# Kernel optimization log

Measured on AMD Instinct MI355X. Metric: run time of the kernel, lower is better.

Reference implementation:

```python
import jax, jax.numpy as jnp
import numpy as np


def setup_inputs() -> dict:
    key = jax.random.key(0)
    k = jax.random.split(key, 6)
    B, S, L, V = 512, 256, 128, 32000
    words = jax.random.randint(k[0], (B, S), 0, V)
    encoder_emits = jax.random.normal(k[1], (B, S, L), dtype=jnp.float32)
    mask = jnp.ones((B, S), dtype=bool)  # token 0 always valid; all-valid lengths here
    feature_table = jax.random.normal(k[2], (V, L), dtype=jnp.float32)
    start = jax.random.normal(k[3], (L,), dtype=jnp.float32)
    transitions = jax.random.normal(k[4], (L, L), dtype=jnp.float32)
    end = jax.random.normal(k[5], (L,), dtype=jnp.float32)
    return {"words": words, "encoder_emits": encoder_emits, "mask": mask,
            "feature_table": feature_table, "start": start,
            "transitions": transitions, "end": end}


def reference(words, encoder_emits, mask, feature_table, start, transitions, end):
    # decoder emits: feature_scorer(words) modeled as per-word label-score lookup
    dec = feature_table[words]                       # [B, S, L]
    # init at t = 0
    log_alpha = start[None, :] + encoder_emits[:, 0]  # [B, L]
    log_beta = log_alpha + dec[:, 0]                  # [B, L]

    def step(carry, xs):
        la, lb = carry
        e_i, d_i, m_i = xs                            # [B,L], [B,L], [B]
        crf = e_i[:, None, :] + transitions[None]     # [B, L, L] (prev, cur)
        a_new = jax.nn.logsumexp(la[:, :, None] + crf, axis=1)
        b_new = jax.nn.logsumexp(lb[:, :, None] + crf + d_i[:, None, :], axis=1)
        m = m_i[:, None]
        return (jnp.where(m, a_new, la), jnp.where(m, b_new, lb)), None

    xs = (jnp.swapaxes(encoder_emits[:, 1:], 0, 1),   # [S-1, B, L]
          jnp.swapaxes(dec[:, 1:], 0, 1),
          mask[:, 1:].T)                              # [S-1, B]
    (log_alpha, log_beta), _ = jax.lax.scan(step, (log_alpha, log_beta), xs)

    la = jax.nn.logsumexp(log_alpha + end[None, :], axis=-1)  # [B]
    lb = jax.nn.logsumexp(log_beta + end[None, :], axis=-1)   # [B]
    return (la - lb).sum()
```

## Files before the change

### kernel.cpp

```cpp
#include <hip/hip_runtime.h>


constexpr int SS  = 256;
constexpr int LL  = 128;
constexpr int BST = 136;

typedef _Float16 half2_t __attribute__((ext_vector_type(2)));
typedef _Float16 half4_t __attribute__((ext_vector_type(4)));
typedef _Float16 half8_t __attribute__((ext_vector_type(8)));
typedef float    f32x4   __attribute__((ext_vector_type(4)));
typedef unsigned uint2_t __attribute__((ext_vector_type(2)));

#define MFMA16(a, b, c) __builtin_amdgcn_mfma_f32_16x16x32_f16((a), (b), (c), 0, 0, 0)
#define PKRTZ(a, b) __builtin_bit_cast(half2_t, __builtin_amdgcn_cvt_pkrtz((a), (b)))

#define BAR() do {                                                \
    asm volatile("s_waitcnt lgkmcnt(0)" ::: "memory");            \
    __builtin_amdgcn_s_barrier();                                 \
    asm volatile("" ::: "memory");                                \
} while (0)

__device__ __forceinline__ float quad_allmax(float x) {
#if __has_builtin(__builtin_amdgcn_permlane16_swap) && __has_builtin(__builtin_amdgcn_permlane32_swap)
    unsigned u = __builtin_bit_cast(unsigned, x);
    uint2_t a = __builtin_amdgcn_permlane16_swap(u, u, false, false);
    float m = fmaxf(__builtin_bit_cast(float, a.x), __builtin_bit_cast(float, a.y));
    unsigned v = __builtin_bit_cast(unsigned, m);
    uint2_t b = __builtin_amdgcn_permlane32_swap(v, v, false, false);
    return fmaxf(__builtin_bit_cast(float, b.x), __builtin_bit_cast(float, b.y));
#else
    x = fmaxf(x, __shfl_xor(x, 16, 64));
    return fmaxf(x, __shfl_xor(x, 32, 64));
#endif
}

__global__ __launch_bounds__(256) void prepass(
    const int* __restrict__ words, const float* __restrict__ emits,
    const float* __restrict__ ftab,
    half4_t* __restrict__ xe, half4_t* __restrict__ xb,
    float* __restrict__ out)
{
    if (blockIdx.x == 0 && threadIdx.x == 0) *out = 0.f;
    const int t = threadIdx.x;
    const int R = blockIdx.x * 8 + (t >> 5);
    const int c = t & 31;
    const int w = words[R];
    const f32x4 e = *(const f32x4*)&emits[(size_t)R * LL + 4 * c];
    const f32x4 d = *(const f32x4*)&ftab[(size_t)w * LL + 4 * c];
    half4_t a, bb;
    #pragma unroll
    for (int r = 0; r < 4; ++r) {
        a[r]  = (_Float16)__expf(e[r]);
        bb[r] = (_Float16)__expf(e[r] + d[r]);
    }
    xe[(size_t)R * 32 + c] = a;
    xb[(size_t)R * 32 + c] = bb;
}

#define STEP(i, XS) do {                                                      \
    const int rp_ = ((i) + 1) & 1, wp_ = (i) & 1;                             \
    O2 -= __log2f(invp);             \
    half8_t bf_[4];                                                           \
    _Pragma("unroll")                                                         \
    for (int c = 0; c < 4; ++c)                                               \
        bf_[c] = *(const half8_t*)&P[rp_][m15 * BST + c * 32 + quad * 8];     \
    f32x4 a0_ = MFMA16(areg[0][0], bf_[0], zero4);                            \
    f32x4 b0_ = MFMA16(areg[0][2], bf_[2], zero4);                            \
    f32x4 a1_ = MFMA16(areg[1][0], bf_[0], zero4);                            \
    f32x4 b1_ = MFMA16(areg[1][2], bf_[2], zero4);                            \
    a0_ = MFMA16(areg[0][1], bf_[1], a0_);                                    \
    b0_ = MFMA16(areg[0][3], bf_[3], b0_);                                    \
    a1_ = MFMA16(areg[1][1], bf_[1], a1_);                                    \
    b1_ = MFMA16(areg[1][3], bf_[3], b1_);                                    \
    const f32x4 y0_ = a0_ + b0_;                                              \
    const f32x4 y1_ = a1_ + b1_;                                              \
    const float p0_ = y0_[0] * (float)XS[0][0] * invp;                        \
    const float p1_ = y0_[1] * (float)XS[0][1] * invp;                        \
    const float p2_ = y0_[2] * (float)XS[0][2] * invp;                        \
    const float p3_ = y0_[3] * (float)XS[0][3] * invp;                        \
    const float q0_ = y1_[0] * (float)XS[1][0] * invp;                        \
    const float q1_ = y1_[1] * (float)XS[1][1] * invp;                        \
    const float q2_ = y1_[2] * (float)XS[1][2] * invp;                        \
    const float q3_ = y1_[3] * (float)XS[1][3] * invp;                        \
    {                                                                         \
        half2_t h0_ = PKRTZ(p0_, p1_), h1_ = PKRTZ(p2_, p3_);                 \
        half4_t pa_; pa_[0]=h0_[0]; pa_[1]=h0_[1]; pa_[2]=h1_[0]; pa_[3]=h1_[1];\
        *(half4_t*)&P[wp_][m15 * BST + t0 * 16 + col0] = pa_;                 \
        half2_t g0_ = PKRTZ(q0_, q1_), g1_ = PKRTZ(q2_, q3_);                 \
        half4_t pb_; pb_[0]=g0_[0]; pb_[1]=g0_[1]; pb_[2]=g1_[0]; pb_[3]=g1_[1];\
        *(half4_t*)&P[wp_][m15 * BST + (t0 + 1) * 16 + col0] = pb_;           \
    }                                                                         \
    const int ipf_ = ((i) + 3 < SS) ? (i) + 3 : SS - 1;                       \
    XS[0] = *(const half4_t*)&X[xrow + (size_t)ipf_ * LL + t0 * 16 + col0];   \
    XS[1] = *(const half4_t*)&X[xrow + (size_t)ipf_ * LL + (t0+1) * 16 + col0];\
    float mm_ = fmaxf(fmaxf(fmaxf(p0_, p1_), fmaxf(p2_, p3_)),               \
                      fmaxf(fmaxf(q0_, q1_), fmaxf(q2_, q3_)));               \
    mm_ = quad_allmax(mm_);                                                   \
    if (quad == 0) PM[wp_][m15][wave] = mm_;                                  \
    BAR();                                                                    \
    const f32x4 pm_ = *(const f32x4*)&PM[wp_][m15][0];                        \
    invp = __builtin_amdgcn_rcpf(fmaxf(fmaxf(pm_[0], pm_[1]),                 \
                                       fmaxf(pm_[2], pm_[3])));               \
} while (0)

__global__ __launch_bounds__(256, 1) void crf_scan(
    const float* __restrict__ start,
    const float* __restrict__ trans,
    const float* __restrict__ endv,
    const _Float16* __restrict__ xe,
    const _Float16* __restrict__ xb,
    float* __restrict__ out)
{
    const int blk   = blockIdx.x;
    const int chain = blk & 1;
    const int grp   = blk >> 1;
    const int tid   = threadIdx.x;
    const int wave  = tid >> 6;
    const int lane  = tid & 63;
    const int m15   = lane & 15;
    const int quad  = lane >> 4;
    const int col0  = quad * 4;
    const int batch = grp * 16 + m15;
    const int t0    = wave * 2;
    const _Float16* __restrict__ X = chain ? xb : xe;

    __shared__ __align__(16) _Float16 P[2][16 * BST];
    __shared__ __align__(16) float    PM[2][16][4];

    half8_t areg[2][4];
    #pragma unroll
    for (int u = 0; u < 2; ++u)
        #pragma unroll
        for (int c = 0; c < 4; ++c)
            #pragma unroll
            for (int jj = 0; jj < 8; ++jj)
                areg[u][c][jj] = (_Float16)__expf(
                    trans[(c * 32 + quad * 8 + jj) * LL + (t0 + u) * 16 + m15]);

    const size_t xrow = (size_t)batch * SS * LL;
    const f32x4 zero4 = (f32x4){0.f, 0.f, 0.f, 0.f};

    float invp, O2 = 0.f;

    {
        float mm = -3.0e38f;
        #pragma unroll
        for (int u = 0; u < 2; ++u) {
            const int s0 = (t0 + u) * 16 + col0;
            const f32x4  sv = *(const f32x4*)&start[s0];
            const half4_t x0 = *(const half4_t*)&X[xrow + s0];
            float y0 = __expf(sv[0]) * (float)x0[0];
            float y1 = __expf(sv[1]) * (float)x0[1];
            float y2 = __expf(sv[2]) * (float)x0[2];
            float y3 = __expf(sv[3]) * (float)x0[3];
            half2_t h0 = PKRTZ(y0, y1), h1 = PKRTZ(y2, y3);
            half4_t pa; pa[0]=h0[0]; pa[1]=h0[1]; pa[2]=h1[0]; pa[3]=h1[1];
            *(half4_t*)&P[0][m15 * BST + s0] = pa;
            mm = fmaxf(mm, fmaxf(fmaxf(y0, y1), fmaxf(y2, y3)));
        }
        mm = quad_allmax(mm);
        if (quad == 0) PM[0][m15][wave] = mm;
    }
    BAR();
    {
        const f32x4 pm = *(const f32x4*)&PM[0][m15][0];
        invp = __builtin_amdgcn_rcpf(fmaxf(fmaxf(pm[0], pm[1]),
                                           fmaxf(pm[2], pm[3])));
    }

    half4_t xA[2], xB[2], xC[2];
    #pragma unroll
    for (int u = 0; u < 2; ++u) {
        xA[u] = *(const half4_t*)&X[xrow + (size_t)1 * LL + (t0+u) * 16 + col0];
        xB[u] = *(const half4_t*)&X[xrow + (size_t)2 * LL + (t0+u) * 16 + col0];
        xC[u] = *(const half4_t*)&X[xrow + (size_t)3 * LL + (t0+u) * 16 + col0];
    }

    for (int i = 1; i + 2 < SS; i += 3) {
        STEP(i,     xA);
        STEP(i + 1, xB);
        STEP(i + 2, xC);
    }

    if (wave == 0) {
        float s = 0.f;
        #pragma unroll
        for (int t = 0; t < 8; ++t) {
            const half4_t p  = *(const half4_t*)&P[1][m15 * BST + t * 16 + col0];
            const f32x4   ev = *(const f32x4*)&endv[t * 16 + col0];
            #pragma unroll
            for (int r = 0; r < 4; ++r)
                s += (float)p[r] * __expf(ev[r]);
        }
        s += __shfl_xor(s, 16, 64);
        s += __shfl_xor(s, 32, 64);
        float lf = O2 * 0.6931471805599453f + __logf(s);
        if (chain) lf = -lf;
        if (quad == 0) {
            lf += __shfl_xor(lf, 1, 64);
            lf += __shfl_xor(lf, 2, 64);
            lf += __shfl_xor(lf, 4, 64);
            lf += __shfl_xor(lf, 8, 64);
            if (m15 == 0) atomicAdd(out, lf);
        }
    }
}

extern "C" void kernel_launch(void* const* d_in, const int* in_sizes, int n_in,
                              void* d_out, int out_size, void* d_ws, size_t ws_size,
                              hipStream_t stream) {
    const int*   words = (const int*)d_in[0];
    const float* emits = (const float*)d_in[1];
    const float* ftab  = (const float*)d_in[3];
    const float* start = (const float*)d_in[4];
    const float* trans = (const float*)d_in[5];
    const float* endv  = (const float*)d_in[6];
    float* out = (float*)d_out;

    half4_t* xe = (half4_t*)d_ws;
    half4_t* xb = xe + (size_t)512 * SS * 32;

    prepass<<<512 * SS / 8, 256, 0, stream>>>(words, emits, ftab, xe, xb, out);
    crf_scan<<<64, 256, 0, stream>>>(start, trans, endv,
                                     (const _Float16*)xe, (const _Float16*)xb, out);
}
```

Baseline: 216.8 us.

## Spread each scan step over eight waves with one output tile per wave

The CRF scan block grows from 4 to 8 waves, so each wave computes one 16-column output tile instead of two. This halves the MFMA chain and the elementwise work per wave on the serial per-step critical path. The per-step max reduction now reads 8 partial maxima from shared memory. The cost is more waves joining each per-step barrier, while the kernel still runs only 64 blocks.

```diff
diff --git a/kernel.cpp b/kernel.cpp
--- a/kernel.cpp
+++ b/kernel.cpp
@@ -64,46 +64,34 @@
     _Pragma("unroll")                                                         \
     for (int c = 0; c < 4; ++c)                                               \
         bf_[c] = *(const half8_t*)&P[rp_][m15 * BST + c * 32 + quad * 8];     \
-    f32x4 a0_ = MFMA16(areg[0][0], bf_[0], zero4);                            \
-    f32x4 b0_ = MFMA16(areg[0][2], bf_[2], zero4);                            \
-    f32x4 a1_ = MFMA16(areg[1][0], bf_[0], zero4);                            \
-    f32x4 b1_ = MFMA16(areg[1][2], bf_[2], zero4);                            \
-    a0_ = MFMA16(areg[0][1], bf_[1], a0_);                                    \
-    b0_ = MFMA16(areg[0][3], bf_[3], b0_);                                    \
-    a1_ = MFMA16(areg[1][1], bf_[1], a1_);                                    \
-    b1_ = MFMA16(areg[1][3], bf_[3], b1_);                                    \
-    const f32x4 y0_ = a0_ + b0_;                                              \
-    const f32x4 y1_ = a1_ + b1_;                                              \
-    const float p0_ = y0_[0] * (float)XS[0][0] * invp;                        \
-    const float p1_ = y0_[1] * (float)XS[0][1] * invp;                        \
-    const float p2_ = y0_[2] * (float)XS[0][2] * invp;                        \
-    const float p3_ = y0_[3] * (float)XS[0][3] * invp;                        \
-    const float q0_ = y1_[0] * (float)XS[1][0] * invp;                        \
-    const float q1_ = y1_[1] * (float)XS[1][1] * invp;                        \
-    const float q2_ = y1_[2] * (float)XS[1][2] * invp;                        \
-    const float q3_ = y1_[3] * (float)XS[1][3] * invp;                        \
+    f32x4 a_ = MFMA16(areg[0], bf_[0], zero4);                                \
+    f32x4 b_ = MFMA16(areg[2], bf_[2], zero4);                                \
+    a_ = MFMA16(areg[1], bf_[1], a_);                                         \
+    b_ = MFMA16(areg[3], bf_[3], b_);                                         \
+    const f32x4 y_ = a_ + b_;                                                 \
+    const float p0_ = y_[0] * (float)XS[0] * invp;                            \
+    const float p1_ = y_[1] * (float)XS[1] * invp;                            \
+    const float p2_ = y_[2] * (float)XS[2] * invp;                            \
+    const float p3_ = y_[3] * (float)XS[3] * invp;                            \
     {                                                                         \
         half2_t h0_ = PKRTZ(p0_, p1_), h1_ = PKRTZ(p2_, p3_);                 \
         half4_t pa_; pa_[0]=h0_[0]; pa_[1]=h0_[1]; pa_[2]=h1_[0]; pa_[3]=h1_[1];\
-        *(half4_t*)&P[wp_][m15 * BST + t0 * 16 + col0] = pa_;                 \
-        half2_t g0_ = PKRTZ(q0_, q1_), g1_ = PKRTZ(q2_, q3_);                 \
-        half4_t pb_; pb_[0]=g0_[0]; pb_[1]=g0_[1]; pb_[2]=g1_[0]; pb_[3]=g1_[1];\
-        *(half4_t*)&P[wp_][m15 * BST + (t0 + 1) * 16 + col0] = pb_;           \
+        *(half4_t*)&P[wp_][m15 * BST + wave * 16 + col0] = pa_;               \
     }                                                                         \
     const int ipf_ = ((i) + 3 < SS) ? (i) + 3 : SS - 1;                       \
-    XS[0] = *(const half4_t*)&X[xrow + (size_t)ipf_ * LL + t0 * 16 + col0];   \
-    XS[1] = *(const half4_t*)&X[xrow + (size_t)ipf_ * LL + (t0+1) * 16 + col0];\
-    float mm_ = fmaxf(fmaxf(fmaxf(p0_, p1_), fmaxf(p2_, p3_)),               \
-                      fmaxf(fmaxf(q0_, q1_), fmaxf(q2_, q3_)));               \
+    XS = *(const half4_t*)&X[xrow + (size_t)ipf_ * LL + wave * 16 + col0];    \
+    float mm_ = fmaxf(fmaxf(p0_, p1_), fmaxf(p2_, p3_));                      \
     mm_ = quad_allmax(mm_);                                                   \
     if (quad == 0) PM[wp_][m15][wave] = mm_;                                  \
     BAR();                                                                    \
-    const f32x4 pm_ = *(const f32x4*)&PM[wp_][m15][0];                        \
-    invp = __builtin_amdgcn_rcpf(fmaxf(fmaxf(pm_[0], pm_[1]),                 \
-                                       fmaxf(pm_[2], pm_[3])));               \
+    const f32x4 pmA_ = *(const f32x4*)&PM[wp_][m15][0];                       \
+    const f32x4 pmB_ = *(const f32x4*)&PM[wp_][m15][4];                       \
+    invp = __builtin_amdgcn_rcpf(                                             \
+        fmaxf(fmaxf(fmaxf(pmA_[0], pmA_[1]), fmaxf(pmA_[2], pmA_[3])),        \
+              fmaxf(fmaxf(pmB_[0], pmB_[1]), fmaxf(pmB_[2], pmB_[3]))));      \
 } while (0)
 
-__global__ __launch_bounds__(256, 1) void crf_scan(
+__global__ __launch_bounds__(512, 1) void crf_scan(
     const float* __restrict__ start,
     const float* __restrict__ trans,
     const float* __restrict__ endv,
@@ -121,21 +109,18 @@
     const int quad  = lane >> 4;
     const int col0  = quad * 4;
     const int batch = grp * 16 + m15;
-    const int t0    = wave * 2;
     const _Float16* __restrict__ X = chain ? xb : xe;
 
     __shared__ __align__(16) _Float16 P[2][16 * BST];
-    __shared__ __align__(16) float    PM[2][16][4];
-
-    half8_t areg[2][4];
+    __shared__ __align__(16) float    PM[2][16][8];
+
+    half8_t areg[4];
     #pragma unroll
-    for (int u = 0; u < 2; ++u)
+    for (int c = 0; c < 4; ++c)
         #pragma unroll
-        for (int c = 0; c < 4; ++c)
-            #pragma unroll
-            for (int jj = 0; jj < 8; ++jj)
-                areg[u][c][jj] = (_Float16)__expf(
-                    trans[(c * 32 + quad * 8 + jj) * LL + (t0 + u) * 16 + m15]);
+        for (int jj = 0; jj < 8; ++jj)
+            areg[c][jj] = (_Float16)__expf(
+                trans[(c * 32 + quad * 8 + jj) * LL + wave * 16 + m15]);
 
     const size_t xrow = (size_t)batch * SS * LL;
     const f32x4 zero4 = (f32x4){0.f, 0.f, 0.f, 0.f};
@@ -143,38 +128,33 @@
     float invp, O2 = 0.f;
 
     {
-        float mm = -3.0e38f;
-        #pragma unroll
-        for (int u = 0; u < 2; ++u) {
-            const int s0 = (t0 + u) * 16 + col0;
-            const f32x4  sv = *(const f32x4*)&start[s0];
-            const half4_t x0 = *(const half4_t*)&X[xrow + s0];
-            float y0 = __expf(sv[0]) * (float)x0[0];
-            float y1 = __expf(sv[1]) * (float)x0[1];
-            float y2 = __expf(sv[2]) * (float)x0[2];
-            float y3 = __expf(sv[3]) * (float)x0[3];
-            half2_t h0 = PKRTZ(y0, y1), h1 = PKRTZ(y2, y3);
-            half4_t pa; pa[0]=h0[0]; pa[1]=h0[1]; pa[2]=h1[0]; pa[3]=h1[1];
-            *(half4_t*)&P[0][m15 * BST + s0] = pa;
-            mm = fmaxf(mm, fmaxf(fmaxf(y0, y1), fmaxf(y2, y3)));
-        }
+        const int s0 = wave * 16 + col0;
+        const f32x4  sv = *(const f32x4*)&start[s0];
+        const half4_t x0 = *(const half4_t*)&X[xrow + s0];
+        float y0 = __expf(sv[0]) * (float)x0[0];
+        float y1 = __expf(sv[1]) * (float)x0[1];
+        float y2 = __expf(sv[2]) * (float)x0[2];
+        float y3 = __expf(sv[3]) * (float)x0[3];
+        half2_t h0 = PKRTZ(y0, y1), h1 = PKRTZ(y2, y3);
+        half4_t pa; pa[0]=h0[0]; pa[1]=h0[1]; pa[2]=h1[0]; pa[3]=h1[1];
+        *(half4_t*)&P[0][m15 * BST + s0] = pa;
+        float mm = fmaxf(fmaxf(y0, y1), fmaxf(y2, y3));
         mm = quad_allmax(mm);
         if (quad == 0) PM[0][m15][wave] = mm;
     }
     BAR();
     {
-        const f32x4 pm = *(const f32x4*)&PM[0][m15][0];
-        invp = __builtin_amdgcn_rcpf(fmaxf(fmaxf(pm[0], pm[1]),
-                                           fmaxf(pm[2], pm[3])));
-    }
-
-    half4_t xA[2], xB[2], xC[2];
-    #pragma unroll
-    for (int u = 0; u < 2; ++u) {
-        xA[u] = *(const half4_t*)&X[xrow + (size_t)1 * LL + (t0+u) * 16 + col0];
-        xB[u] = *(const half4_t*)&X[xrow + (size_t)2 * LL + (t0+u) * 16 + col0];
-        xC[u] = *(const half4_t*)&X[xrow + (size_t)3 * LL + (t0+u) * 16 + col0];
-    }
+        const f32x4 pmA = *(const f32x4*)&PM[0][m15][0];
+        const f32x4 pmB = *(const f32x4*)&PM[0][m15][4];
+        invp = __builtin_amdgcn_rcpf(
+            fmaxf(fmaxf(fmaxf(pmA[0], pmA[1]), fmaxf(pmA[2], pmA[3])),
+                  fmaxf(fmaxf(pmB[0], pmB[1]), fmaxf(pmB[2], pmB[3]))));
+    }
+
+    half4_t xA, xB, xC;
+    xA = *(const half4_t*)&X[xrow + (size_t)1 * LL + wave * 16 + col0];
+    xB = *(const half4_t*)&X[xrow + (size_t)2 * LL + wave * 16 + col0];
+    xC = *(const half4_t*)&X[xrow + (size_t)3 * LL + wave * 16 + col0];
 
     for (int i = 1; i + 2 < SS; i += 3) {
         STEP(i,     xA);
@@ -221,6 +201,6 @@
     half4_t* xb = xe + (size_t)512 * SS * 32;
 
     prepass<<<512 * SS / 8, 256, 0, stream>>>(words, emits, ftab, xe, xb, out);
-    crf_scan<<<64, 256, 0, stream>>>(start, trans, endv,
+    crf_scan<<<64, 512, 0, stream>>>(start, trans, endv,
                                      (const _Float16*)xe, (const _Float16*)xb, out);
 }
```

Measured after the change: 222.1 us. 2.4% more time.
